# Kernel optimization log

Measured on AMD Instinct MI355X. Metric: run time of the kernel, lower is better.

## Reference

```python
import jax, jax.numpy as jnp
import numpy as np

V, D, H = 5000, 300, 256
B, T = 16, 512


def setup_inputs() -> dict:
    key = jax.random.key(0)
    ks = jax.random.split(key, 14)
    def w(k, shape):
        return jax.random.normal(k, shape, dtype=jnp.float32) * 0.02
    return {
        "x": jax.random.normal(ks[0], (B, T, V), dtype=jnp.float32),
        "hidden_state": jax.random.normal(ks[1], (1, H), dtype=jnp.float32),
        "context_state": jax.random.normal(ks[2], (1, H), dtype=jnp.float32),
        "E": w(ks[3], (D, V)),      # embedding Linear weight [out,in]
        "Wf": w(ks[4], (H, D)), "Uf": w(ks[5], (H, H)),
        "Wg": w(ks[6], (H, D)), "Ug": w(ks[7], (H, H)),
        "Wi": w(ks[8], (H, D)), "Ui": w(ks[9], (H, H)),
        "Wo": w(ks[10], (H, D)), "Uo": w(ks[11], (H, H)),
        "Wout": w(ks[12], (V, H)),
    }


def reference(x, hidden_state, context_state, E, Wf, Uf, Wg, Ug, Wi, Ui, Wo, Uo, Wout):
    # Precompute all input-side projections in one batched pass: [B,T,D]
    emb = jnp.einsum('btv,dv->btd', x, E)
    # Stack input-gate GEMMs: [B,T,4H]
    Wx = jnp.concatenate([Wf, Wg, Wi, Wo], axis=0)  # [4H, D]
    gates_x = jnp.einsum('btd,gd->btg', emb, Wx)    # [B, T, 4H]
    Uh = jnp.concatenate([Uf, Ug, Ui, Uo], axis=0)  # [4H, H]

    h0 = jnp.broadcast_to(hidden_state, (x.shape[0], hidden_state.shape[-1]))
    c0 = jnp.broadcast_to(context_state, (x.shape[0], context_state.shape[-1]))

    Hn = hidden_state.shape[-1]

    def step(carry, gx):
        h, c = carry
        gh = h @ Uh.T                     # [B, 4H]
        z = gx + gh
        f = jax.nn.sigmoid(z[:, 0*Hn:1*Hn])
        g = jnp.tanh(z[:, 1*Hn:2*Hn])
        i = jax.nn.sigmoid(z[:, 2*Hn:3*Hn])
        o = jax.nn.sigmoid(z[:, 3*Hn:4*Hn])
        c_new = g * i + c * f
        h_new = o * jnp.tanh(c_new)
        # NOTE: faithful to source - output projects g, not h
        out = g @ Wout.T                  # [B, V]
        return (h_new, c_new), out

    _, outs = jax.lax.scan(step, (h0, c0), jnp.swapaxes(gates_x, 0, 1))
    return jnp.swapaxes(outs, 0, 1)       # [B, T, V]
```

## Files before the change

### kernel.cpp

```cpp
#include <hip/hip_runtime.h>
#include <stdint.h>

typedef unsigned short u16;
typedef unsigned int u32;
typedef __attribute__((ext_vector_type(8))) __bf16 bf16x8;
typedef __attribute__((ext_vector_type(4))) float f32x4;
typedef __attribute__((ext_vector_type(4))) u32 u32x4;
typedef __attribute__((ext_vector_type(2))) u32 u32x2;
typedef __attribute__((ext_vector_type(4))) int i32x4;

#define DEV __device__ __forceinline__

constexpr int V = 5000, D = 300, H = 256, BB = 16, T = 512;
constexpr int M = BB * T;
constexpr int DP = 320;
constexpr int KP = 5024;
constexpr int G4 = 1024;
constexpr int NPAD = 5120;

constexpr size_t OFF_EB    = 0;
constexpr size_t OFF_WXB   = OFF_EB    + (size_t)DP * KP * 2;
constexpr size_t OFF_UHB   = OFF_WXB   + (size_t)G4 * DP * 2;
constexpr size_t OFF_WOUTB = OFF_UHB   + (size_t)G4 * H * 2;
constexpr size_t OFF_GATES = OFF_WOUTB + (size_t)NPAD * H * 2;
constexpr size_t OFF_GALL  = OFF_GATES + (size_t)T * BB * G4 * 2;

DEV u16 f2bf(float f) {
  u32 i = __builtin_bit_cast(u32, f);
  return (u16)((i + 0x7FFFu + ((i >> 16) & 1u)) >> 16);
}
DEV float bf2f(u16 u) { return __builtin_bit_cast(float, (u32)u << 16); }
DEV f32x4 MFMA(u32x4 a, u32x4 b, f32x4 c) {
  return __builtin_amdgcn_mfma_f32_16x16x32_bf16(
      __builtin_bit_cast(bf16x8, a), __builtin_bit_cast(bf16x8, b), c, 0, 0, 0);
}
DEV i32x4 MFMA8(u32x4 a, u32x4 b, i32x4 c) {
  return __builtin_amdgcn_mfma_i32_16x16x64_i8(
      __builtin_bit_cast(i32x4, a), __builtin_bit_cast(i32x4, b), c, 0, 0, 0);
}
DEV float sigm(float x) { return 1.f / (1.f + __expf(-x)); }
DEV float tanh_s(float x) { float e = __expf(2.f * x); return 1.f - 2.f / (e + 1.f); }

DEV void bar_lds() {
  asm volatile("s_waitcnt lgkmcnt(0)" ::: "memory");
  __builtin_amdgcn_sched_barrier(0);
  __builtin_amdgcn_s_barrier();
  __builtin_amdgcn_sched_barrier(0);
}

__global__ __launch_bounds__(256) void k_prep(
    const float* __restrict__ E, const float* __restrict__ Wf, const float* __restrict__ Wg,
    const float* __restrict__ Wi, const float* __restrict__ Wo,
    const float* __restrict__ Uf, const float* __restrict__ Ug,
    const float* __restrict__ Ui, const float* __restrict__ Uo,
    const float* __restrict__ Wout, char* __restrict__ ws) {
  if (blockIdx.x >= 1024) {
    char* qU = ws + OFF_UHB;
    float* zsc = (float*)(ws + OFF_UHB + (size_t)G4 * H);
    const int row = (blockIdx.x - 1024) * 4 + (threadIdx.x >> 6);
    const int lane = threadIdx.x & 63;
    const float* Up = (row < 256) ? Uf : (row < 512) ? Ug : (row < 768) ? Ui : Uo;
    f32x4 v = *(const f32x4*)(Up + (size_t)(row & 255) * H + lane * 4);
    float m = fmaxf(fmaxf(fabsf(v[0]), fabsf(v[1])), fmaxf(fabsf(v[2]), fabsf(v[3])));
    for (int i = 1; i < 64; i <<= 1) m = fmaxf(m, __shfl_xor(m, i));
    float inv = (m > 0.f) ? 127.f / m : 0.f;
    int q0 = (int)rintf(v[0] * inv), q1 = (int)rintf(v[1] * inv);
    int q2 = (int)rintf(v[2] * inv), q3 = (int)rintf(v[3] * inv);
    q0 = max(-127, min(127, q0)); q1 = max(-127, min(127, q1));
    q2 = max(-127, min(127, q2)); q3 = max(-127, min(127, q3));
    u32 pk = (u32)(q0 & 255) | ((u32)(q1 & 255) << 8) | ((u32)(q2 & 255) << 16) |
             ((u32)(q3 & 255) << 24);
    *(u32*)(qU + (size_t)row * H + lane * 4) = pk;
    if (lane == 0) zsc[row] = m / 16129.f;
    return;
  }
  u16* Eb = (u16*)(ws + OFF_EB);
  u16* Wxb = (u16*)(ws + OFF_WXB);
  u16* Wob = (u16*)(ws + OFF_WOUTB);
  const int NE = DP * KP, NW = G4 * DP, NWO = NPAD * H;
  const int total = NE + NW + NWO;
  for (int i = blockIdx.x * blockDim.x + threadIdx.x; i < total; i += 1024 * blockDim.x) {
    int j = i;
    if (j < NE) {
      int nn = j / KP, k = j % KP;
      Eb[j] = f2bf((nn < D && k < V) ? E[(size_t)nn * V + k] : 0.f);
      continue;
    }
    j -= NE;
    if (j < NW) {
      int r = j / DP, k = j % DP;
      const float* Wp = (r < 256) ? Wf : (r < 512) ? Wg : (r < 768) ? Wi : Wo;
      Wxb[j] = f2bf((k < D) ? Wp[(size_t)(r & 255) * D + k] : 0.f);
      continue;
    }
    j -= NW;
    if (j < NWO) {
      int nn = j / H, k = j % H;
      Wob[j] = f2bf((nn < V) ? Wout[(size_t)nn * H + k] : 0.f);
      continue;
    }
  }
}

__global__ __launch_bounds__(512) void k_embgates(const float* __restrict__ x,
                                                  char* __restrict__ ws) {
  __shared__ __align__(16) char sm[50688];
  u16* As = (u16*)sm;
  u16* Bs = (u16*)(sm + 4608);
  u16* embS = (u16*)sm;
  const u16* Eb = (const u16*)(ws + OFF_EB);
  const u16* Wxb = (const u16*)(ws + OFF_WXB);
  u16* gates = (u16*)(ws + OFF_GATES);

  const int tid = threadIdx.x;
  const int lane = tid & 63, wv = tid >> 6;
  const int l15 = lane & 15, lc = lane >> 4;
  const int it = blockIdx.x;
  const int tc = it >> 4, b = it & 15;
  const int m0x = b * T + tc * 32;

  f32x4 acc[5];
#pragma unroll
  for (int j = 0; j < 5; j++) acc[j] = (f32x4){0.f, 0.f, 0.f, 0.f};
  const int ar = tid >> 4, ak = (tid & 15) * 4;
  f32x4 xv0, xv1;
  u32x4 ev0[5], ev1[5];

#define WEMB_ISSUE(SFX, KS)                                                       \
  do {                                                                            \
    int k0_ = (KS) * 64;                                                          \
    {                                                                             \
      size_t base_ = (size_t)(m0x + ar) * V + k0_ + ak;                           \
      if (k0_ + ak + 3 < V) {                                                     \
        xv##SFX = *(const f32x4*)(x + base_);                                     \
      } else {                                                                    \
        f32x4 t_;                                                                 \
        t_[0] = (k0_ + ak + 0 < V) ? x[base_ + 0] : 0.f;                          \
        t_[1] = (k0_ + ak + 1 < V) ? x[base_ + 1] : 0.f;                          \
        t_[2] = (k0_ + ak + 2 < V) ? x[base_ + 2] : 0.f;                          \
        t_[3] = (k0_ + ak + 3 < V) ? x[base_ + 3] : 0.f;                          \
        xv##SFX = t_;                                                             \
      }                                                                           \
    }                                                                             \
    _Pragma("unroll") for (int p_ = 0; p_ < 5; p_++) {                            \
      int cc_ = tid + 512 * p_;                                                   \
      int n_ = cc_ >> 3, ko_ = (cc_ & 7) * 8;                                     \
      ev##SFX[p_] = *(const u32x4*)(Eb + (size_t)n_ * KP + k0_ + ko_);            \
    }                                                                             \
  } while (0)

#define WEMB_WRITE(SFX)                                                           \
  do {                                                                            \
    {                                                                             \
      union { u16 u[4]; u32x2 v; } ua_;                                           \
      ua_.u[0] = f2bf(xv##SFX[0]); ua_.u[1] = f2bf(xv##SFX[1]);                   \
      ua_.u[2] = f2bf(xv##SFX[2]); ua_.u[3] = f2bf(xv##SFX[3]);                   \
      *(u32x2*)&As[ar * 72 + ak] = ua_.v;                                         \
    }                                                                             \
    _Pragma("unroll") for (int p_ = 0; p_ < 5; p_++) {                            \
      int cc_ = tid + 512 * p_;                                                   \
      int n_ = cc_ >> 3, ko_ = (cc_ & 7) * 8;                                     \
      *(u32x4*)&Bs[n_ * 72 + ko_] = ev##SFX[p_];                                  \
    }                                                                             \
  } while (0)

  const int mt = wv & 1, ntb = (wv >> 1) * 5;
  auto wemb_compute = [&]() {
#pragma unroll
    for (int ksub = 0; ksub < 2; ksub++) {
      u32x4 a = *(const u32x4*)&As[(mt * 16 + l15) * 72 + ksub * 32 + lc * 8];
#pragma unroll
      for (int j = 0; j < 5; j++) {
        u32x4 bb = *(const u32x4*)&Bs[((ntb + j) * 16 + l15) * 72 + ksub * 32 + lc * 8];
        acc[j] = MFMA(a, bb, acc[j]);
      }
    }
  };

  constexpr int NK = 79;
  WEMB_ISSUE(0, 0);
  WEMB_ISSUE(1, 1);
  for (int ks = 0; ks < NK; ks += 2) {
    __syncthreads();
    WEMB_WRITE(0);
    if (ks + 2 < NK) WEMB_ISSUE(0, ks + 2);
    __syncthreads();
    wemb_compute();
    if (ks + 1 < NK) {
      __syncthreads();
      WEMB_WRITE(1);
      if (ks + 3 < NK) WEMB_ISSUE(1, ks + 3);
      __syncthreads();
      wemb_compute();
    }
  }
#undef WEMB_ISSUE
#undef WEMB_WRITE
  __syncthreads();
#pragma unroll
  for (int j = 0; j < 5; j++) {
    int nn = (ntb + j) * 16 + l15;
#pragma unroll
    for (int r = 0; r < 4; r++)
      embS[(mt * 16 + lc * 4 + r) * 328 + nn] = f2bf(acc[j][r]);
  }
  __syncthreads();

  const int amt = wv & 1, ngrp = wv >> 1;
  f32x4 gacc[16];
#pragma unroll
  for (int j = 0; j < 16; j++) gacc[j] = (f32x4){0.f, 0.f, 0.f, 0.f};
#pragma unroll 1
  for (int kc = 0; kc < 10; kc++) {
    u32x4 a = *(const u32x4*)&embS[(amt * 16 + l15) * 328 + kc * 32 + lc * 8];
#pragma unroll
    for (int nt = 0; nt < 16; nt++) {
      int col = ngrp * 256 + nt * 16 + l15;
      u32x4 bb = *(const u32x4*)(Wxb + (size_t)col * DP + kc * 32 + lc * 8);
      gacc[nt] = MFMA(a, bb, gacc[nt]);
    }
  }
#pragma unroll
  for (int nt = 0; nt < 16; nt++) {
#pragma unroll
    for (int r = 0; r < 4; r++) {
      int t = tc * 32 + amt * 16 + lc * 4 + r;
      int col = ngrp * 256 + nt * 16 + l15;
      int q = col >> 8, nn = col & 255;
      gates[(((size_t)t * 16 + b) * 256 + nn) * 4 + q] = f2bf(gacc[nt][r]);
    }
  }
}

__global__ __launch_bounds__(512) void k_scan(const float* __restrict__ hidden,
                                              const float* __restrict__ ctx,
                                              char* __restrict__ ws) {
  const char* qU = (const char*)(ws + OFF_UHB);
  const float* zsc = (const float*)(ws + OFF_UHB + (size_t)G4 * H);
  const u16* gates = (const u16*)(ws + OFF_GATES);
  u16* gall = (u16*)(ws + OFF_GALL);

  __shared__ __align__(16) char pq[2][2][256];
  __shared__ __align__(16) int zw[2][8][8][2][16];

  const int tid = threadIdx.x;
  const int lane = tid & 63, wv = tid >> 6;
  const int l15 = lane & 15, lc = lane >> 4;

  u32x4 uq[4][2][4];
#pragma unroll
  for (int gg = 0; gg < 4; gg++)
#pragma unroll
    for (int j = 0; j < 2; j++)
#pragma unroll
      for (int kt = 0; kt < 4; kt++)
        uq[gg][j][kt] = *(const u32x4*)(
            qU + (size_t)(gg * 256 + wv * 32 + j * 16 + l15) * H + kt * 64 + lc * 16);

  const int b = lane >> 5, np = lane & 31;
  const int n = wv * 32 + np;
  const int jj = (np >> 4) & 1, rr = np & 15;
  const int b_glob = blockIdx.x * 2 + b;
  float c = ctx[n];
  const float zs0 = zsc[n], zs1 = zsc[n + 256], zs2 = zsc[n + 512], zs3 = zsc[n + 768];
  u32x2 gxc = *(const u32x2*)(gates + (((size_t)0 * 16 + b_glob) * 256 + n) * 4);
  u32x2 gxn = *(const u32x2*)(gates + (((size_t)1 * 16 + b_glob) * 256 + n) * 4);
  const u16* gxp = gates + (((size_t)2 * 16 + b_glob) * 256 + n) * 4;
  u16* gallp = gall + (size_t)b_glob * T * H + n;

  {
    const int b0 = tid >> 8, n0i = tid & 255;
    float h0 = hidden[n0i];
    h0 = fminf(3.999f, fmaxf(-3.999f, h0));
    pq[0][b0][n0i] = (char)(int)rintf(h0 * 31.75f);
  }
  __syncthreads();

#define SCAN_STEP(PAR, S0, S1, S2, S3)                                                     \
  {                                                                                        \
    u32x4 bfr[4];                                                                          \
    _Pragma("unroll") for (int kt = 0; kt < 4; kt++)                                       \
        bfr[kt] = *(const u32x4*)&pq[PAR][l15 & 1][kt * 64 + lc * 16];                     \
    i32x4 acc[4][2];                                                                       \
    _Pragma("unroll") for (int gg = 0; gg < 4; gg++)                                       \
        _Pragma("unroll") for (int j = 0; j < 2; j++) {                                    \
      i32x4 a = {0, 0, 0, 0};                                                              \
      _Pragma("unroll") for (int kt = 0; kt < 4; kt++)                                     \
          a = MFMA8(uq[gg][j][kt], bfr[kt], a);                                            \
      acc[gg][j] = a;                                                                      \
    }                                                                                      \
    if (l15 < 2) {                                                                         \
      _Pragma("unroll") for (int gg = 0; gg < 4; gg++)                                     \
          _Pragma("unroll") for (int j = 0; j < 2; j++)                                    \
              *(i32x4*)&zw[PAR][wv][gg * 2 + j][l15][lc * 4] = acc[gg][j];                 \
    }                                                                                      \
    asm volatile("s_waitcnt lgkmcnt(0)" ::: "memory");                                     \
    __builtin_amdgcn_sched_barrier(0);                                                     \
    float z0 = (float)zw[PAR][wv][0 + jj][b][rr] * (S0) + bf2f((u16)(gxc[0] & 0xFFFFu));   \
    float z1 = (float)zw[PAR][wv][2 + jj][b][rr] * (S1) + bf2f((u16)(gxc[0] >> 16));       \
    float z2 = (float)zw[PAR][wv][4 + jj][b][rr] * (S2) + bf2f((u16)(gxc[1] & 0xFFFFu));   \
    float z3 = (float)zw[PAR][wv][6 + jj][b][rr] * (S3) + bf2f((u16)(gxc[1] >> 16));       \
    float fv = sigm(z0), gv = tanh_s(z1), iv = sigm(z2), ov = sigm(z3);                    \
    c = gv * iv + c * fv;                                                                  \
    float hn = ov * tanh_s(c);                                                             \
    *gallp = f2bf(gv);                                                                     \
    gallp += H;                                                                            \
    pq[(PAR) ^ 1][b][n] = (char)(int)rintf(hn * 127.f);                                    \
    gxc = gxn;                                                                             \
    gxn = *(const u32x2*)gxp;                                                              \
    gxp += 16384;                                                  \
    bar_lds();                                                                             \
  }

  SCAN_STEP(0, zs0 * 4.f, zs1 * 4.f, zs2 * 4.f, zs3 * 4.f)
#pragma unroll 1
  for (int t = 1; t + 1 < T; t += 2) {
    SCAN_STEP(1, zs0, zs1, zs2, zs3)
    SCAN_STEP(0, zs0, zs1, zs2, zs3)
  }
  SCAN_STEP(1, zs0, zs1, zs2, zs3)
#undef SCAN_STEP
}

__global__ __launch_bounds__(256) void k_out(char* __restrict__ ws, float* __restrict__ out) {
  const u16* gall = (const u16*)(ws + OFF_GALL);
  const u16* Wob = (const u16*)(ws + OFF_WOUTB);
  __shared__ __align__(16) u16 As[64 * 40];
  __shared__ __align__(16) u16 Bs[256 * 40];
  __shared__ __align__(16) float tb[64 * 132];

  const int tid = threadIdx.x;
  const int blk = blockIdx.x;
  const int m0 = (blk / 20) * 64, n0 = (blk % 20) * 256;
  const int lane = tid & 63, wv = tid >> 6;
  const int l15 = lane & 15, lc = lane >> 4;

  f32x4 acc[16];
#pragma unroll
  for (int j = 0; j < 16; j++) acc[j] = (f32x4){0.f, 0.f, 0.f, 0.f};

  u32x4 av0, av1;
  u32x4 bv0[4], bv1[4];

#define OUT_ISSUE(SFX, KS)                                                        \
  do {                                                                            \
    int k0_ = (KS) * 32;                                                          \
    {                                                                             \
      int r_ = tid >> 2, ko_ = (tid & 3) * 8;                                     \
      av##SFX = *(const u32x4*)(gall + (size_t)(m0 + r_) * H + k0_ + ko_);        \
    }                                                                             \
    _Pragma("unroll") for (int j_ = 0; j_ < 4; j_++) {                            \
      int c_ = tid + 256 * j_;                                                    \
      int n_ = c_ >> 2, ko_ = (c_ & 3) * 8;                                       \
      bv##SFX[j_] = *(const u32x4*)(Wob + (size_t)(n0 + n_) * H + k0_ + ko_);     \
    }                                                                             \
  } while (0)

#define OUT_WRITE(SFX)                                                            \
  do {                                                                            \
    {                                                                             \
      int r_ = tid >> 2, ko_ = (tid & 3) * 8;                                     \
      *(u32x4*)&As[r_ * 40 + ko_] = av##SFX;                                      \
    }                                                                             \
    _Pragma("unroll") for (int j_ = 0; j_ < 4; j_++) {                            \
      int c_ = tid + 256 * j_;                                                    \
      int n_ = c_ >> 2, ko_ = (c_ & 3) * 8;                                       \
      *(u32x4*)&Bs[n_ * 40 + ko_] = bv##SFX[j_];                                  \
    }                                                                             \
  } while (0)

  auto out_compute = [&]() {
    u32x4 a = *(const u32x4*)&As[(wv * 16 + l15) * 40 + lc * 8];
#pragma unroll
    for (int nt = 0; nt < 16; nt++) {
      u32x4 b = *(const u32x4*)&Bs[(nt * 16 + l15) * 40 + lc * 8];
      acc[nt] = MFMA(a, b, acc[nt]);
    }
  };

  constexpr int NK = 8;
  OUT_ISSUE(0, 0);
  OUT_ISSUE(1, 1);
  for (int ks = 0; ks < NK; ks += 2) {
    __syncthreads();
    OUT_WRITE(0);
    if (ks + 2 < NK) OUT_ISSUE(0, ks + 2);
    __syncthreads();
    out_compute();
    __syncthreads();
    OUT_WRITE(1);
    if (ks + 3 < NK) OUT_ISSUE(1, ks + 3);
    __syncthreads();
    out_compute();
  }

#pragma unroll
  for (int h = 0; h < 2; h++) {
    __syncthreads();
#pragma unroll
    for (int nt = 0; nt < 8; nt++) {
#pragma unroll
      for (int r = 0; r < 4; r++)
        tb[(wv * 16 + lc * 4 + r) * 132 + nt * 16 + l15] = acc[h * 8 + nt][r];
    }
    __syncthreads();
#pragma unroll
    for (int cc = 0; cc < 8; cc++) {
      int idx = cc * 256 + tid;
      int row = idx >> 5, c4 = (idx & 31) * 4;
      int gcol = n0 + h * 128 + c4;
      if (gcol + 3 < V) {
        f32x4 v = *(const f32x4*)&tb[row * 132 + c4];
        *(f32x4*)&out[(size_t)(m0 + row) * V + gcol] = v;
      }
    }
  }
#undef OUT_ISSUE
#undef OUT_WRITE
}

extern "C" void kernel_launch(void* const* d_in, const int* in_sizes, int n_in,
                              void* d_out, int out_size, void* d_ws, size_t ws_size,
                              hipStream_t stream) {
  (void)in_sizes; (void)n_in; (void)out_size; (void)ws_size;
  const float* x      = (const float*)d_in[0];
  const float* hidden = (const float*)d_in[1];
  const float* ctx    = (const float*)d_in[2];
  const float* E      = (const float*)d_in[3];
  const float* Wf     = (const float*)d_in[4];
  const float* Uf     = (const float*)d_in[5];
  const float* Wg     = (const float*)d_in[6];
  const float* Ug     = (const float*)d_in[7];
  const float* Wi     = (const float*)d_in[8];
  const float* Ui     = (const float*)d_in[9];
  const float* Wo     = (const float*)d_in[10];
  const float* Uo     = (const float*)d_in[11];
  const float* Wout   = (const float*)d_in[12];
  char* ws = (char*)d_ws;
  float* out = (float*)d_out;

  hipLaunchKernelGGL(k_prep, dim3(1280), dim3(256), 0, stream,
                     E, Wf, Wg, Wi, Wo, Uf, Ug, Ui, Uo, Wout, ws);
  hipLaunchKernelGGL(k_embgates, dim3(256), dim3(512), 0, stream, x, ws);
  hipLaunchKernelGGL(k_scan, dim3(8), dim3(512), 0, stream, hidden, ctx, ws);
  hipLaunchKernelGGL(k_out, dim3((M / 64) * 20), dim3(256), 0, stream, ws, out);
}
```

Before: 726.0 us.

## Load output-GEMM fragments directly from global memory, drop LDS staging

The output projection kernel no longer stages A and B tiles through shared memory with double-buffered register prefetch and barriers. Each wave now loads its A fragments for all K once into registers and streams B fragments directly from global memory into the MFMA for each N tile. This removes the LDS writes, reads and the syncs in the K loop. In exchange the four waves each re-read the same Wout tile from global/L2 without LDS sharing, the loads are less coalesced (16-byte chunks spaced by row stride), and register pressure rises.

```diff
diff --git a/kernel.cpp b/kernel.cpp
--- a/kernel.cpp
+++ b/kernel.cpp
@@ -325,8 +325,6 @@
 __global__ __launch_bounds__(256) void k_out(char* __restrict__ ws, float* __restrict__ out) {
   const u16* gall = (const u16*)(ws + OFF_GALL);
   const u16* Wob = (const u16*)(ws + OFF_WOUTB);
-  __shared__ __align__(16) u16 As[64 * 40];
-  __shared__ __align__(16) u16 Bs[256 * 40];
   __shared__ __align__(16) float tb[64 * 132];
 
   const int tid = threadIdx.x;
@@ -339,59 +337,19 @@
 #pragma unroll
   for (int j = 0; j < 16; j++) acc[j] = (f32x4){0.f, 0.f, 0.f, 0.f};
 
-  u32x4 av0, av1;
-  u32x4 bv0[4], bv1[4];
-
-#define OUT_ISSUE(SFX, KS)                                                        \
-  do {                                                                            \
-    int k0_ = (KS) * 32;                                                          \
-    {                                                                             \
-      int r_ = tid >> 2, ko_ = (tid & 3) * 8;                                     \
-      av##SFX = *(const u32x4*)(gall + (size_t)(m0 + r_) * H + k0_ + ko_);        \
-    }                                                                             \
-    _Pragma("unroll") for (int j_ = 0; j_ < 4; j_++) {                            \
-      int c_ = tid + 256 * j_;                                                    \
-      int n_ = c_ >> 2, ko_ = (c_ & 3) * 8;                                       \
-      bv##SFX[j_] = *(const u32x4*)(Wob + (size_t)(n0 + n_) * H + k0_ + ko_);     \
-    }                                                                             \
-  } while (0)
-
-#define OUT_WRITE(SFX)                                                            \
-  do {                                                                            \
-    {                                                                             \
-      int r_ = tid >> 2, ko_ = (tid & 3) * 8;                                     \
-      *(u32x4*)&As[r_ * 40 + ko_] = av##SFX;                                      \
-    }                                                                             \
-    _Pragma("unroll") for (int j_ = 0; j_ < 4; j_++) {                            \
-      int c_ = tid + 256 * j_;                                                    \
-      int n_ = c_ >> 2, ko_ = (c_ & 3) * 8;                                       \
-      *(u32x4*)&Bs[n_ * 40 + ko_] = bv##SFX[j_];                                  \
-    }                                                                             \
-  } while (0)
-
-  auto out_compute = [&]() {
-    u32x4 a = *(const u32x4*)&As[(wv * 16 + l15) * 40 + lc * 8];
-#pragma unroll
-    for (int nt = 0; nt < 16; nt++) {
-      u32x4 b = *(const u32x4*)&Bs[(nt * 16 + l15) * 40 + lc * 8];
-      acc[nt] = MFMA(a, b, acc[nt]);
-    }
-  };
-
-  constexpr int NK = 8;
-  OUT_ISSUE(0, 0);
-  OUT_ISSUE(1, 1);
-  for (int ks = 0; ks < NK; ks += 2) {
-    __syncthreads();
-    OUT_WRITE(0);
-    if (ks + 2 < NK) OUT_ISSUE(0, ks + 2);
-    __syncthreads();
-    out_compute();
-    __syncthreads();
-    OUT_WRITE(1);
-    if (ks + 3 < NK) OUT_ISSUE(1, ks + 3);
-    __syncthreads();
-    out_compute();
+  u32x4 afr[8];
+  const u16* ga = gall + (size_t)(m0 + wv * 16 + l15) * H + lc * 8;
+#pragma unroll
+  for (int ks = 0; ks < 8; ks++) afr[ks] = *(const u32x4*)(ga + ks * 32);
+
+#pragma unroll
+  for (int nt = 0; nt < 16; nt++) {
+    const u16* wb = Wob + (size_t)(n0 + nt * 16 + l15) * H + lc * 8;
+#pragma unroll
+    for (int ks = 0; ks < 8; ks++) {
+      u32x4 bfr = *(const u32x4*)(wb + ks * 32);
+      acc[nt] = MFMA(afr[ks], bfr, acc[nt]);
+    }
   }
 
 #pragma unroll
@@ -415,8 +373,6 @@
       }
     }
   }
-#undef OUT_ISSUE
-#undef OUT_WRITE
 }
 
 extern "C" void kernel_launch(void* const* d_in, const int* in_sizes, int n_in,
```

Result: slower. 860.2 us (+18.5%).
